# Kernel tuning notes

Hardware: AMD Instinct MI355X
Metric: run time of the kernel (lower is better)

## Reference

```python
import jax, jax.numpy as jnp
import numpy as np

BN_EPS = 1e-5

def _conv(x, w, b, pad):
    # x: [B,C,H,W], w: [O,I,kh,kw] -> [B,O,H,W]
    y = jax.lax.conv_general_dilated(x, w, window_strides=(1, 1),
                                     padding=[(pad, pad), (pad, pad)],
                                     dimension_numbers=("NCHW", "OIHW", "NCHW"))
    return y + b[None, :, None, None]

def setup_inputs() -> dict:
    key = jax.random.key(0)
    ks = jax.random.split(key, 5)
    B, Cin, H, W = 2, 256, 80, 80
    Ck, Cv, Cout = 128, 256, 256
    std = 0.02  # matches torch normal_(0, 0.02) init
    return {
        "x": jax.random.normal(ks[0], (B, Cin, H, W), jnp.float32),
        "wk": std * jax.random.normal(ks[1], (Ck, Cin, 1, 1), jnp.float32),
        "bk": jnp.zeros((Ck,), jnp.float32),
        "gamma": jnp.ones((Ck,), jnp.float32),
        "beta": jnp.zeros((Ck,), jnp.float32),
        "rmean": jnp.zeros((Ck,), jnp.float32),
        "rvar": jnp.ones((Ck,), jnp.float32),
        "wv": std * jax.random.normal(ks[2], (Cv, Cin, 3, 3), jnp.float32),
        "bv": jnp.zeros((Cv,), jnp.float32),
        "ww": std * jax.random.normal(ks[3], (Cout, Cv, 1, 1), jnp.float32),
        "bw": jnp.zeros((Cout,), jnp.float32),
    }

def reference(x, wk, bk, gamma, beta, rmean, rvar, wv, bv, ww, bw):
    B, Cin, H, W = x.shape
    Ck, Cv = wk.shape[0], wv.shape[0]
    N = H * W

    # f_key == f_query (shared module): 1x1 conv + BatchNorm (inference stats)
    kq = _conv(x, wk, bk, pad=0)                      # [B,Ck,H,W]
    inv = gamma / jnp.sqrt(rvar + BN_EPS)
    kq = kq * inv[None, :, None, None] + (beta - rmean * inv)[None, :, None, None]
    kq = kq.reshape(B, Ck, N)                          # key layout [B,Ck,N]

    # f_value: 3x3 conv
    value = _conv(x, wv, bv, pad=1).reshape(B, Cv, N)  # [B,Cv,N]

    # sim_map = query^T @ key -> [B,N,N], full softmax over last dim
    sim = jnp.einsum("bcn,bcm->bnm", kq, kq)
    sim = jax.nn.softmax(sim, axis=-1)

    # context = sim @ value^T -> [B,N,Cv] -> [B,Cv,H,W]
    ctx = jnp.einsum("bnm,bcm->bcn", sim, value).reshape(B, Cv, H, W)

    out = _conv(ctx, ww, bw, pad=0) + x                # residual
    return out
```

## Files before the change

### kernel.cpp

```cpp
#include <hip/hip_runtime.h>
#include <math.h>

#define NB   2
#define CIN  256
#define IMH  80
#define IMW  80
#define NPIX (IMH*IMW)
#define CK   128
#define CVC  256
#define COUTC 256
#define BN_EPS 1e-5f
#define HP   82
#define WP   82
#define NMC  (NPIX / 64)
#define LOG2E 1.4426950408889634f
#define M0L  28.853900817779268f

typedef short sx8 __attribute__((ext_vector_type(8)));
typedef short sx4 __attribute__((ext_vector_type(4)));
typedef float f32x4 __attribute__((ext_vector_type(4)));

__device__ __forceinline__ short f2bf(float f) {
    unsigned u = __builtin_bit_cast(unsigned, f);
    u += 0x7fffu + ((u >> 16) & 1u);
    return (short)(u >> 16);
}
__device__ __forceinline__ float bf2f(short s) {
    unsigned u = ((unsigned)(unsigned short)s) << 16;
    return __builtin_bit_cast(float, u);
}
__device__ __forceinline__ int pk_bf16(float a, float b) {
    unsigned ua = __builtin_bit_cast(unsigned, a) + 0x8000u;
    unsigned ub = __builtin_bit_cast(unsigned, b) + 0x8000u;
    return __builtin_amdgcn_perm(ub, ua, 0x07060302);
}

__global__ __launch_bounds__(256) void pad_kernel(const float* __restrict__ x,
                                                  short* __restrict__ xpad)
{
    __shared__ short T[64][258];
    const int tid = threadIdx.x;
    const int n0  = blockIdx.x * 64;
    const int b   = blockIdx.y;
    const float* xb = x + (size_t)b * CIN * NPIX;

    #pragma unroll 4
    for (int i = 0; i < 64; ++i) {
        int e = tid + i * 256;
        int pix = e & 63, c = e >> 6;
        T[pix][c] = f2bf(xb[(size_t)c * NPIX + n0 + pix]);
    }
    __syncthreads();
    #pragma unroll
    for (int i = 0; i < 8; ++i) {
        int e   = tid + i * 256;
        int pix = e >> 5;
        int cp  = (e & 31) * 8;
        int np  = n0 + pix;
        int hp  = np / IMW + 1, wp = np % IMW + 1;
        sx8 v = *(const sx8*)&T[pix][cp];
        *(sx8*)&xpad[(((size_t)b * HP + hp) * WP + wp) * CIN + cp] = v;
    }
}

__global__ __launch_bounds__(256) void wvt_kernel(const float* __restrict__ wv,
                                                  short* __restrict__ wvt)
{
    int idx = blockIdx.x * 256 + threadIdx.x;
    int tap = idx >> 16;
    int cv  = (idx >> 8) & 255;
    int c   = idx & 255;
    wvt[idx] = f2bf(wv[((size_t)cv * CIN + c) * 9 + tap]);
}

__global__ __launch_bounds__(256) void wwb_kernel(const float* __restrict__ ww,
                                                  short* __restrict__ wwb)
{
    int idx = blockIdx.x * 256 + threadIdx.x;
    wwb[idx] = f2bf(ww[idx]);
}

__global__ __launch_bounds__(256) void wkb_kernel(
    const float* __restrict__ wk, const float* __restrict__ bk,
    const float* __restrict__ gamma, const float* __restrict__ beta,
    const float* __restrict__ rmean, const float* __restrict__ rvar,
    short* __restrict__ wkb, float* __restrict__ bias2)
{
    int idx = blockIdx.x * 256 + threadIdx.x;
    int ck = idx >> 8;
    float inv = gamma[ck] * rsqrtf(rvar[ck] + BN_EPS);
    wkb[idx] = f2bf(wk[idx] * inv);
    if (idx < CK) {
        float invi = gamma[idx] * rsqrtf(rvar[idx] + BN_EPS);
        bias2[idx] = (bk[idx] - rmean[idx]) * invi + beta[idx];
    }
}

__global__ __launch_bounds__(256) void kq_kernel(
    const short* __restrict__ xpad, const short* __restrict__ wkb,
    const float* __restrict__ bias2, short* __restrict__ kqT)
{
    __shared__ short T[64][136];
    const int tid  = threadIdx.x;
    const int wid  = tid >> 6;
    const int lane = tid & 63;
    const int l15  = lane & 15;
    const int quad = lane >> 4;
    const int n0 = blockIdx.x * 64;
    const int b  = blockIdx.y;
    const short* xb = xpad + (size_t)b * HP * WP * CIN;
    const int ck0 = wid * 32;

    const short* brow[4];
    #pragma unroll
    for (int nt = 0; nt < 4; ++nt) {
        int n = n0 + nt * 16 + l15;
        int hp = n / IMW + 1, wp = n % IMW + 1;
        brow[nt] = xb + ((size_t)hp * WP + wp) * CIN;
    }

    f32x4 acc[2][4];
    #pragma unroll
    for (int at = 0; at < 2; ++at)
        #pragma unroll
        for (int nt = 0; nt < 4; ++nt)
            acc[at][nt] = (f32x4){0.f, 0.f, 0.f, 0.f};

    for (int kc = 0; kc < CIN / 32; ++kc) {
        sx8 af0 = *(const sx8*)&wkb[(size_t)(ck0 + l15) * CIN + kc * 32 + quad * 8];
        sx8 af1 = *(const sx8*)&wkb[(size_t)(ck0 + 16 + l15) * CIN + kc * 32 + quad * 8];
        #pragma unroll
        for (int nt = 0; nt < 4; ++nt) {
            sx8 bf = *(const sx8*)&brow[nt][kc * 32 + quad * 8];
            acc[0][nt] = __builtin_amdgcn_mfma_f32_16x16x32_bf16(af0, bf, acc[0][nt], 0, 0, 0);
            acc[1][nt] = __builtin_amdgcn_mfma_f32_16x16x32_bf16(af1, bf, acc[1][nt], 0, 0, 0);
        }
    }

    #pragma unroll
    for (int at = 0; at < 2; ++at) {
        f32x4 b4 = *(const f32x4*)&bias2[ck0 + at * 16 + quad * 4];
        #pragma unroll
        for (int nt = 0; nt < 4; ++nt)
            #pragma unroll
            for (int r = 0; r < 4; ++r)
                T[nt * 16 + l15][ck0 + at * 16 + quad * 4 + r] = f2bf(acc[at][nt][r] + b4[r]);
    }
    __syncthreads();
    #pragma unroll
    for (int it = 0; it < 4; ++it) {
        int e = tid + it * 256;
        int row = e >> 4, c8 = (e & 15) * 8;
        *(sx8*)&kqT[((size_t)b * NPIX + n0 + row) * CK + c8] = *(const sx8*)&T[row][c8];
    }
}

#define CSTRIDE 36
__global__ __launch_bounds__(512) void conv3_kernel(
    const short* __restrict__ xpad, const short* __restrict__ wvt,
    const float* __restrict__ bv, short* __restrict__ valF)
{
    __shared__ __align__(16) short Xs[2][6 * 18 * CSTRIDE];

    const int tid  = threadIdx.x;
    const int wid  = tid >> 6;
    const int lane = tid & 63;
    const int l15  = lane & 15;
    const int quad = lane >> 4;

    const int rowT = blockIdx.x / 5, colT = blockIdx.x % 5;
    const int h0 = rowT * 4, w0 = colT * 16;
    const int cv0 = blockIdx.y * 128 + wid * 16;
    const int b   = blockIdx.z;

    const short* xb = xpad + (size_t)b * HP * WP * CIN;

    const int rc  = tid >> 2, l4 = tid & 3;
    const int row = rc / 18, col = rc % 18;
    const bool sv = (tid < 432);
    const short* sptr = &xb[(((size_t)(h0 + row)) * WP + (w0 + col)) * CIN + l4 * 8];
    const int sdst = rc * CSTRIDE + l4 * 8;

    f32x4 acc[4];
    #pragma unroll
    for (int r = 0; r < 4; ++r) acc[r] = (f32x4){0.f, 0.f, 0.f, 0.f};

    sx8 v = {};
    if (sv) {
        v = *(const sx8*)&sptr[0];
        *(sx8*)&Xs[0][sdst] = v;
    }
    __syncthreads();

    for (int cc = 0; cc < CIN / 32; ++cc) {
        const int cur = cc & 1;
        if (cc + 1 < CIN / 32 && sv)
            v = *(const sx8*)&sptr[(cc + 1) * 32];

        #pragma unroll
        for (int dw = 0; dw < 3; ++dw) {
            sx8 Bf[6];
            #pragma unroll
            for (int rr = 0; rr < 6; ++rr)
                Bf[rr] = *(const sx8*)&Xs[cur][(rr * 18 + l15 + dw) * CSTRIDE + quad * 8];
            #pragma unroll
            for (int dh = 0; dh < 3; ++dh) {
                int tap = dh * 3 + dw;
                sx8 Af = *(const sx8*)&wvt[((size_t)(tap * 256 + cv0 + l15)) * CIN + cc * 32 + quad * 8];
                #pragma unroll
                for (int r = 0; r < 4; ++r)
                    acc[r] = __builtin_amdgcn_mfma_f32_16x16x32_bf16(Af, Bf[r + dh], acc[r], 0, 0, 0);
            }
        }

        if (cc + 1 < CIN / 32 && sv)
            *(sx8*)&Xs[cur ^ 1][sdst] = v;
        __syncthreads();
    }

    f32x4 bvv = *(const f32x4*)&bv[cv0 + quad * 4];
    const int cvt = cv0 >> 4;
    #pragma unroll
    for (int r = 0; r < 4; ++r) {
        int n  = (h0 + r) * IMW + w0 + l15;
        int mc = n >> 6, s2 = (n >> 5) & 1, qm = (n >> 3) & 3, mi = n & 7;
        size_t base = ((((size_t)(b * NMC + mc) * 16 + cvt) * 2 + s2) * 4 + qm) * 128;
        #pragma unroll
        for (int reg = 0; reg < 4; ++reg)
            valF[base + (quad * 4 + reg) * 8 + mi] = f2bf(acc[r][reg] + bvv[reg]);
    }
}

#define TQ 64
#define TK 64
#define KS_LD 132
#define PS_LD 72

template<int SP>
__global__ __launch_bounds__(512) void attn_kernel(
    const short* __restrict__ kqT, const short* __restrict__ valF,
    short* __restrict__ opart, float* __restrict__ lpart)
{
    constexpr int NCc  = NPIX / SP / 64;
    constexpr int SPSH = (SP == 4) ? 3 : 2;

    __shared__ __align__(16) short Ks[TK][KS_LD];
    __shared__ __align__(16) short Pb[TQ][PS_LD];
    __shared__ float lqs[2][64];

    const int tid  = threadIdx.x;
    const int wid  = tid >> 6;
    const int lane = tid & 63;
    const int l15  = lane & 15;
    const int quad = lane >> 4;
    const int qw   = wid & 3;
    const int mh   = wid >> 2;

    const int blk = blockIdx.x;
    const int b   = blk & 1;
    const int sp  = (blk >> 1) & (SP - 1);
    const int n0  = (blk >> SPSH) * TQ;
    const int mb  = sp * (NPIX / SP);

    const short* kqb = kqT + (size_t)b * NPIX * CK;
    const short* vbase = valF + ((size_t)(b * NMC + sp * NCc) * 16 + wid * 2) * 1024
                              + (size_t)lane * 8;

    const int srow = tid >> 4;
    const int sc8  = (tid & 15) * 8;

    sx8 qf[4];
    #pragma unroll
    for (int s = 0; s < 4; ++s)
        qf[s] = *(const sx8*)&kqb[(size_t)(n0 + qw * 16 + l15) * CK + s * 32 + quad * 8];

    sx8 kreg[2];
    #pragma unroll
    for (int p = 0; p < 2; ++p)
        kreg[p] = *(const sx8*)&kqb[(size_t)(mb + srow + p * 32) * CK + sc8];
    #pragma unroll
    for (int p = 0; p < 2; ++p)
        *(sx8*)&Ks[srow + p * 32][sc8] = kreg[p];

    sx8 vreg[4];
    #pragma unroll
    for (int ct = 0; ct < 2; ++ct)
        #pragma unroll
        for (int s2 = 0; s2 < 2; ++s2)
            vreg[ct * 2 + s2] = *(const sx8*)&vbase[ct * 1024 + s2 * 512];

    float lq = 0.f;
    f32x4 acc[4][2];
    #pragma unroll
    for (int qt = 0; qt < 4; ++qt)
        #pragma unroll
        for (int ct = 0; ct < 2; ++ct)
            acc[qt][ct] = (f32x4){0.f, 0.f, 0.f, 0.f};

    __syncthreads();

    for (int i = 0; i < NCc; ++i) {
        if (i + 1 < NCc) {
            #pragma unroll
            for (int p = 0; p < 2; ++p)
                kreg[p] = *(const sx8*)&kqb[(size_t)(mb + (i + 1) * TK + srow + p * 32) * CK + sc8];
        }

        f32x4 st[2];
        #pragma unroll
        for (int t2 = 0; t2 < 2; ++t2) st[t2] = (f32x4){0.f, 0.f, 0.f, 0.f};
        #pragma unroll
        for (int s = 0; s < 4; ++s) {
            sx8 af[2];
            #pragma unroll
            for (int t2 = 0; t2 < 2; ++t2)
                af[t2] = *(const sx8*)&Ks[mh * 32 + t2 * 16 + l15][s * 32 + quad * 8];
            #pragma unroll
            for (int t2 = 0; t2 < 2; ++t2)
                st[t2] = __builtin_amdgcn_mfma_f32_16x16x32_bf16(af[t2], qf[s], st[t2], 0, 0, 0);
        }

        __syncthreads();

        #pragma unroll
        for (int t2 = 0; t2 < 2; ++t2)
            #pragma unroll
            for (int r = 0; r < 4; ++r)
                st[t2][r] = exp2f(fmaf(st[t2][r], LOG2E, -M0L));

        if (i + 1 < NCc) {
            #pragma unroll
            for (int p = 0; p < 2; ++p)
                *(sx8*)&Ks[srow + p * 32][sc8] = kreg[p];
        }

        #pragma unroll
        for (int t2 = 0; t2 < 2; ++t2) {
            int2 pw;
            pw.x = pk_bf16(st[t2][0], st[t2][1]);
            pw.y = pk_bf16(st[t2][2], st[t2][3]);
            *(int2*)&Pb[qw * 16 + l15][mh * 32 + t2 * 16 + quad * 4] = pw;
        }

        lq += (st[0][0] + st[0][1]) + (st[0][2] + st[0][3])
            + (st[1][0] + st[1][1]) + (st[1][2] + st[1][3]);

        __syncthreads();

        #pragma unroll
        for (int s2 = 0; s2 < 2; ++s2) {
            sx8 pa[4];
            #pragma unroll
            for (int qt = 0; qt < 4; ++qt)
                pa[qt] = *(const sx8*)&Pb[qt * 16 + l15][s2 * 32 + quad * 8];
            #pragma unroll
            for (int ct = 0; ct < 2; ++ct) {
                #pragma unroll
                for (int qt = 0; qt < 4; ++qt)
                    acc[qt][ct] = __builtin_amdgcn_mfma_f32_16x16x32_bf16(pa[qt], vreg[ct * 2 + s2], acc[qt][ct], 0, 0, 0);
            }
        }

        if (i + 1 < NCc) {
            #pragma unroll
            for (int ct = 0; ct < 2; ++ct)
                #pragma unroll
                for (int s2 = 0; s2 < 2; ++s2)
                    vreg[ct * 2 + s2] = *(const sx8*)&vbase[(size_t)(i + 1) * 16384 + ct * 1024 + s2 * 512];
        }
    }

    lq += __shfl_xor(lq, 16);
    lq += __shfl_xor(lq, 32);
    if (quad == 0)
        lqs[mh][qw * 16 + l15] = lq;

    size_t obase = (size_t)(sp * NB + b) * NPIX + n0;
    #pragma unroll
    for (int qt = 0; qt < 4; ++qt)
        #pragma unroll
        for (int ct = 0; ct < 2; ++ct) {
            int cv = wid * 32 + ct * 16 + l15;
            #pragma unroll
            for (int r = 0; r < 4; ++r)
                opart[(obase + qt * 16 + quad * 4 + r) * CVC + cv] = f2bf(acc[qt][ct][r]);
        }

    __syncthreads();
    if (tid < 64)
        lpart[obase + tid] = lqs[0][tid] + lqs[1][tid];
}

#define BS_LD 40
template<int SP>
__global__ __launch_bounds__(512) void out_kernel(
    const short* __restrict__ opart, const float* __restrict__ lpart,
    const short* __restrict__ wwb, const float* __restrict__ bw,
    const float* __restrict__ x, float* __restrict__ out)
{
    __shared__ __align__(16) short Bs[2][64][BS_LD];
    __shared__ float rinvs[64];

    const int tid  = threadIdx.x;
    const int wid  = tid >> 6;
    const int lane = tid & 63;
    const int l15  = lane & 15;
    const int quad = lane >> 4;

    const int n0  = blockIdx.x * 64;
    const int co0 = blockIdx.y * 128 + wid * 16;
    const int b   = blockIdx.z;

    if (tid < 64) {
        int n = n0 + tid;
        float ls = 0.f;
        #pragma unroll
        for (int s = 0; s < SP; ++s)
            ls += lpart[(size_t)(s * NB + b) * NPIX + n];
        rinvs[tid] = 1.f / ls;
    }

    const int srow = tid >> 2;
    const int sc8  = (tid & 3) * 8;
    const short* op0 = opart + ((size_t)b * NPIX + n0 + srow) * CVC + sc8;
    constexpr size_t SSTR = (size_t)NB * NPIX * CVC;
    const bool sv = (tid < 256);

    __syncthreads();

    if (sv) {
        float ri = rinvs[srow];
        float sacc[8] = {0.f, 0.f, 0.f, 0.f, 0.f, 0.f, 0.f, 0.f};
        #pragma unroll
        for (int s = 0; s < SP; ++s) {
            sx8 a = *(const sx8*)&op0[s * SSTR];
            #pragma unroll
            for (int j = 0; j < 8; ++j)
                sacc[j] += bf2f(a[j]);
        }
        sx8 o;
        #pragma unroll
        for (int j = 0; j < 8; ++j)
            o[j] = f2bf(sacc[j] * ri);
        *(sx8*)&Bs[0][srow][sc8] = o;
    }
    __syncthreads();

    f32x4 acc[4];
    #pragma unroll
    for (int nt = 0; nt < 4; ++nt) acc[nt] = (f32x4){0.f, 0.f, 0.f, 0.f};

    for (int cc = 0; cc < CVC / 32; ++cc) {
        const int cur = cc & 1;
        const bool st = (cc + 1 < CVC / 32) && sv;

        sx8 a[SP];
        if (st) {
            #pragma unroll
            for (int s = 0; s < SP; ++s)
                a[s] = *(const sx8*)&op0[s * SSTR + (cc + 1) * 32];
        }

        sx8 af = *(const sx8*)&wwb[(size_t)(co0 + l15) * CVC + cc * 32 + quad * 8];
        #pragma unroll
        for (int nt = 0; nt < 4; ++nt) {
            sx8 bf = *(const sx8*)&Bs[cur][nt * 16 + l15][quad * 8];
            acc[nt] = __builtin_amdgcn_mfma_f32_16x16x32_bf16(af, bf, acc[nt], 0, 0, 0);
        }

        if (st) {
            float ri = rinvs[srow];
            float sacc[8] = {0.f, 0.f, 0.f, 0.f, 0.f, 0.f, 0.f, 0.f};
            #pragma unroll
            for (int s = 0; s < SP; ++s)
                #pragma unroll
                for (int j = 0; j < 8; ++j)
                    sacc[j] += bf2f(a[s][j]);
            sx8 o;
            #pragma unroll
            for (int j = 0; j < 8; ++j)
                o[j] = f2bf(sacc[j] * ri);
            *(sx8*)&Bs[cur ^ 1][srow][sc8] = o;
        }
        __syncthreads();
    }

    f32x4 bv4 = *(const f32x4*)&bw[co0 + quad * 4];
    #pragma unroll
    for (int nt = 0; nt < 4; ++nt) {
        #pragma unroll
        for (int r = 0; r < 4; ++r) {
            int co = co0 + quad * 4 + r;
            int n  = n0 + nt * 16 + l15;
            size_t gi = ((size_t)b * COUTC + co) * NPIX + n;
            out[gi] = acc[nt][r] + bv4[r] + x[gi];
        }
    }
}

extern "C" void kernel_launch(void* const* d_in, const int* in_sizes, int n_in,
                              void* d_out, int out_size, void* d_ws, size_t ws_size,
                              hipStream_t stream)
{
    const float* x     = (const float*)d_in[0];
    const float* wk    = (const float*)d_in[1];
    const float* bk    = (const float*)d_in[2];
    const float* gamma = (const float*)d_in[3];
    const float* beta  = (const float*)d_in[4];
    const float* rmean = (const float*)d_in[5];
    const float* rvar  = (const float*)d_in[6];
    const float* wv    = (const float*)d_in[7];
    const float* bv    = (const float*)d_in[8];
    const float* ww    = (const float*)d_in[9];
    const float* bw    = (const float*)d_in[10];
    float* out = (float*)d_out;

    const size_t perSplit = (size_t)NB * NPIX * CVC;
    const size_t persistShorts = (size_t)COUTC * CVC + (size_t)CK * CIN
                               + (size_t)NB * NPIX * CK + (size_t)NB * NPIX * CVC;
    const size_t need4 = 2ull * (4ull * perSplit + persistShorts)
                       + 4ull * (CK + 4ull * NB * NPIX);
    const int SPL = (ws_size >= need4) ? 4 : 2;

    short* opart = (short*)d_ws;
    short* xpad  = opart;
    short* wvt   = xpad + (size_t)NB * HP * WP * CIN;
    short* wwb   = opart + (size_t)SPL * perSplit;
    short* wkb   = wwb  + (size_t)COUTC * CVC;
    short* kqT   = wkb  + (size_t)CK * CIN;
    short* valF  = kqT  + (size_t)NB * NPIX * CK;
    float* bias2 = (float*)(valF + perSplit);
    float* lpart = bias2 + CK;

    hipMemsetAsync(xpad, 0, (size_t)NB * HP * WP * CIN * sizeof(short), stream);

    pad_kernel   <<<dim3(NPIX/64, NB),          256, 0, stream>>>(x, xpad);
    wvt_kernel   <<<(9*CVC*CIN)/256,            256, 0, stream>>>(wv, wvt);
    wwb_kernel   <<<(COUTC*CVC)/256,            256, 0, stream>>>(ww, wwb);
    wkb_kernel   <<<(CK*CIN)/256,               256, 0, stream>>>(wk, bk, gamma, beta, rmean, rvar, wkb, bias2);
    kq_kernel    <<<dim3(NPIX/64, NB),          256, 0, stream>>>(xpad, wkb, bias2, kqT);
    conv3_kernel <<<dim3(100, CVC/128,     NB), 512, 0, stream>>>(xpad, wvt, bv, valF);

    if (SPL == 4) {
        attn_kernel<4> <<<NB * 4 * (NPIX / TQ), 512, 0, stream>>>(kqT, valF, opart, lpart);
        out_kernel<4>  <<<dim3(100, COUTC/128, NB), 512, 0, stream>>>(opart, lpart, wwb, bw, x, out);
    } else {
        attn_kernel<2> <<<NB * 2 * (NPIX / TQ), 512, 0, stream>>>(kqT, valF, opart, lpart);
        out_kernel<2>  <<<dim3(100, COUTC/128, NB), 512, 0, stream>>>(opart, lpart, wwb, bw, x, out);
    }
}
```

Measured before the change: 243.3 us.

## Fuse weight prep kernels and merge padding with kq projection

The three weight-conversion kernels are merged into one prep kernel, and the wv transpose now goes through shared memory so its global reads are coalesced. The pad kernel and the kq 1x1-conv kernel are fused, so kq reads its input straight from the shared tile instead of re-reading xpad from global memory. The full-buffer memset is replaced by zeroing only the border pixels inside the fused kernel. Together these cut kernel launches, a large memset and a global round trip, at the cost of a longer fused kernel with more shared-memory use.

```diff
diff --git a/kernel.cpp b/kernel.cpp
--- a/kernel.cpp
+++ b/kernel.cpp
@@ -35,8 +35,51 @@
     return __builtin_amdgcn_perm(ub, ua, 0x07060302);
 }
 
-__global__ __launch_bounds__(256) void pad_kernel(const float* __restrict__ x,
-                                                  short* __restrict__ xpad)
+#define WVT_BLKS 256
+#define WWB_BLKS 256
+#define WKB_BLKS 128
+__global__ __launch_bounds__(256) void prep_kernel(
+    const float* __restrict__ wv, const float* __restrict__ ww,
+    const float* __restrict__ wk, const float* __restrict__ bk,
+    const float* __restrict__ gamma, const float* __restrict__ beta,
+    const float* __restrict__ rmean, const float* __restrict__ rvar,
+    short* __restrict__ wvt, short* __restrict__ wwb,
+    short* __restrict__ wkb, float* __restrict__ bias2)
+{
+    __shared__ short L[9][258];
+    const int tid = threadIdx.x;
+    const int bx  = blockIdx.x;
+
+    if (bx < WVT_BLKS) {
+        const float* src = wv + (size_t)bx * 2304;
+        #pragma unroll
+        for (int i = 0; i < 9; ++i) {
+            int m = i * 256 + tid;
+            L[m % 9][m / 9] = f2bf(src[m]);
+        }
+        __syncthreads();
+        #pragma unroll
+        for (int j = 0; j < 9; ++j)
+            wvt[(size_t)j * (CVC * CIN) + bx * 256 + tid] = L[j][tid];
+    } else if (bx < WVT_BLKS + WWB_BLKS) {
+        int idx = (bx - WVT_BLKS) * 256 + tid;
+        wwb[idx] = f2bf(ww[idx]);
+    } else {
+        int idx = (bx - WVT_BLKS - WWB_BLKS) * 256 + tid;
+        int ck = idx >> 8;
+        float inv = gamma[ck] * rsqrtf(rvar[ck] + BN_EPS);
+        wkb[idx] = f2bf(wk[idx] * inv);
+        if (idx < CK) {
+            float invi = gamma[idx] * rsqrtf(rvar[idx] + BN_EPS);
+            bias2[idx] = (bk[idx] - rmean[idx]) * invi + beta[idx];
+        }
+    }
+}
+
+__global__ __launch_bounds__(256) void padkq_kernel(
+    const float* __restrict__ x, const short* __restrict__ wkb,
+    const float* __restrict__ bias2, short* __restrict__ xpad,
+    short* __restrict__ kqT)
 {
     __shared__ short T[64][258];
     const int tid = threadIdx.x;
@@ -51,6 +94,7 @@
         T[pix][c] = f2bf(xb[(size_t)c * NPIX + n0 + pix]);
     }
     __syncthreads();
+
     #pragma unroll
     for (int i = 0; i < 8; ++i) {
         int e   = tid + i * 256;
@@ -61,63 +105,26 @@
         sx8 v = *(const sx8*)&T[pix][cp];
         *(sx8*)&xpad[(((size_t)b * HP + hp) * WP + wp) * CIN + cp] = v;
     }
-}
-
-__global__ __launch_bounds__(256) void wvt_kernel(const float* __restrict__ wv,
-                                                  short* __restrict__ wvt)
-{
-    int idx = blockIdx.x * 256 + threadIdx.x;
-    int tap = idx >> 16;
-    int cv  = (idx >> 8) & 255;
-    int c   = idx & 255;
-    wvt[idx] = f2bf(wv[((size_t)cv * CIN + c) * 9 + tap]);
-}
-
-__global__ __launch_bounds__(256) void wwb_kernel(const float* __restrict__ ww,
-                                                  short* __restrict__ wwb)
-{
-    int idx = blockIdx.x * 256 + threadIdx.x;
-    wwb[idx] = f2bf(ww[idx]);
-}
-
-__global__ __launch_bounds__(256) void wkb_kernel(
-    const float* __restrict__ wk, const float* __restrict__ bk,
-    const float* __restrict__ gamma, const float* __restrict__ beta,
-    const float* __restrict__ rmean, const float* __restrict__ rvar,
-    short* __restrict__ wkb, float* __restrict__ bias2)
-{
-    int idx = blockIdx.x * 256 + threadIdx.x;
-    int ck = idx >> 8;
-    float inv = gamma[ck] * rsqrtf(rvar[ck] + BN_EPS);
-    wkb[idx] = f2bf(wk[idx] * inv);
-    if (idx < CK) {
-        float invi = gamma[idx] * rsqrtf(rvar[idx] + BN_EPS);
-        bias2[idx] = (bk[idx] - rmean[idx]) * invi + beta[idx];
-    }
-}
-
-__global__ __launch_bounds__(256) void kq_kernel(
-    const short* __restrict__ xpad, const short* __restrict__ wkb,
-    const float* __restrict__ bias2, short* __restrict__ kqT)
-{
-    __shared__ short T[64][136];
-    const int tid  = threadIdx.x;
+
+    {
+        int e = blockIdx.x * 256 + tid;
+        if (e < 324 * 32) {
+            int p = e >> 5, c8 = (e & 31) * 8;
+            int hp, wp;
+            if      (p < 82)  { hp = 0;       wp = p;       }
+            else if (p < 164) { hp = 81;      wp = p - 82;  }
+            else if (p < 244) { hp = p - 163; wp = 0;       }
+            else              { hp = p - 243; wp = 81;      }
+            sx8 z = {};
+            *(sx8*)&xpad[(((size_t)b * HP + hp) * WP + wp) * CIN + c8] = z;
+        }
+    }
+
     const int wid  = tid >> 6;
     const int lane = tid & 63;
     const int l15  = lane & 15;
     const int quad = lane >> 4;
-    const int n0 = blockIdx.x * 64;
-    const int b  = blockIdx.y;
-    const short* xb = xpad + (size_t)b * HP * WP * CIN;
-    const int ck0 = wid * 32;
-
-    const short* brow[4];
-    #pragma unroll
-    for (int nt = 0; nt < 4; ++nt) {
-        int n = n0 + nt * 16 + l15;
-        int hp = n / IMW + 1, wp = n % IMW + 1;
-        brow[nt] = xb + ((size_t)hp * WP + wp) * CIN;
-    }
+    const int ck0  = wid * 32;
 
     f32x4 acc[2][4];
     #pragma unroll
@@ -131,11 +138,13 @@
         sx8 af1 = *(const sx8*)&wkb[(size_t)(ck0 + 16 + l15) * CIN + kc * 32 + quad * 8];
         #pragma unroll
         for (int nt = 0; nt < 4; ++nt) {
-            sx8 bf = *(const sx8*)&brow[nt][kc * 32 + quad * 8];
+            sx8 bf = *(const sx8*)&T[nt * 16 + l15][kc * 32 + quad * 8];
             acc[0][nt] = __builtin_amdgcn_mfma_f32_16x16x32_bf16(af0, bf, acc[0][nt], 0, 0, 0);
             acc[1][nt] = __builtin_amdgcn_mfma_f32_16x16x32_bf16(af1, bf, acc[1][nt], 0, 0, 0);
         }
     }
+
+    __syncthreads();
 
     #pragma unroll
     for (int at = 0; at < 2; ++at) {
@@ -532,13 +541,9 @@
     float* bias2 = (float*)(valF + perSplit);
     float* lpart = bias2 + CK;
 
-    hipMemsetAsync(xpad, 0, (size_t)NB * HP * WP * CIN * sizeof(short), stream);
-
-    pad_kernel   <<<dim3(NPIX/64, NB),          256, 0, stream>>>(x, xpad);
-    wvt_kernel   <<<(9*CVC*CIN)/256,            256, 0, stream>>>(wv, wvt);
-    wwb_kernel   <<<(COUTC*CVC)/256,            256, 0, stream>>>(ww, wwb);
-    wkb_kernel   <<<(CK*CIN)/256,               256, 0, stream>>>(wk, bk, gamma, beta, rmean, rvar, wkb, bias2);
-    kq_kernel    <<<dim3(NPIX/64, NB),          256, 0, stream>>>(xpad, wkb, bias2, kqT);
+    prep_kernel  <<<WVT_BLKS + WWB_BLKS + WKB_BLKS, 256, 0, stream>>>(
+        wv, ww, wk, bk, gamma, beta, rmean, rvar, wvt, wwb, wkb, bias2);
+    padkq_kernel <<<dim3(NPIX/64, NB),          256, 0, stream>>>(x, wkb, bias2, xpad, kqT);
     conv3_kernel <<<dim3(100, CVC/128,     NB), 512, 0, stream>>>(xpad, wvt, bv, valF);
 
     if (SPL == 4) {
```

New measurement: 231.6 us. -4.8%, faster.
